# Kernel tuning notes

Measured on AMD Instinct MI355X. Metric: run time of the kernel, lower is better.

Reference implementation:

```python
import jax, jax.numpy as jnp
import numpy as np

TIMESTEPS = 1000
DIFFUSION_SPEED = 0.01
B, N = 4, 2048
E = N * (N - 1) // 2  # strict lower-triangular entries per graph


def _build_Qt():
    # Qt[t-1] = [[1-f, f], [f, 1-f]],  f = 0.5*(1-(1-2s)^t), t = 1..T
    ts = jnp.arange(1, TIMESTEPS + 1, dtype=jnp.float32)
    flip = 0.5 * (1.0 - (1.0 - 2.0 * DIFFUSION_SPEED) ** ts)          # [T]
    row0 = jnp.stack([1.0 - flip, flip], axis=-1)                      # [T,2]
    row1 = jnp.stack([flip, 1.0 - flip], axis=-1)                      # [T,2]
    return jnp.stack([row0, row1], axis=1)                             # [T,2,2]


def setup_inputs() -> dict:
    key = jax.random.key(0)
    k1, k2, k3, k4 = jax.random.split(key, 4)
    adj_start = jax.random.randint(k1, (B, N, N), 0, 2, dtype=jnp.int32)
    t = jax.random.randint(k2, (B,), 0, TIMESTEPS, dtype=jnp.int32)
    u = jax.random.uniform(k3, (B, N, N), dtype=jnp.float32)
    q_approx = jax.random.normal(k4, (B, E), dtype=jnp.float32)
    return {"adj_start": adj_start, "t": t, "u": u, "q_approx": q_approx}


def reference(adj_start, t, u, q_approx):
    Qt = _build_Qt()                                                   # [T,2,2]
    # symmetrize raw adjacency into a binary undirected adjacency
    a = jnp.tril(adj_start, -1)
    adj0 = a + jnp.swapaxes(a, -1, -2)                                 # [B,N,N] in {0,1}

    b_idx = jnp.arange(B)[:, None, None]

    # ---- forward diffusion: sample x_t ~ Categorical(Qt[t][adj0]) ----
    probs = Qt[t][b_idx, adj0]                                         # [B,N,N,2]
    x_t = (u < probs[..., 1]).astype(adj0.dtype)                       # [B,N,N]

    # ---- backward diffusion: q(x_{t-1} | x_t, x_0) ----
    Q_likelihood = Qt[0]                                               # [2,2]
    Q_prior = Qt[t - 1]                                                # [B,2,2] (t=0 wraps, as in torch)
    Q_evidence = Qt[t]                                                 # [B,2,2]

    likelihood = Q_likelihood[x_t]                                     # [B,N,N,2]
    prior = Q_prior[b_idx, adj0]                                       # [B,N,N,2]
    evidence = Q_evidence[b_idx, adj0, x_t]                            # [B,N,N]
    q_backward = likelihood * prior / evidence[..., None]              # [B,N,N,2]

    ti, tj = np.tril_indices(N, -1)                                    # static indices
    q_target = q_backward[:, ti, tj, 1]                                # [B,E]

    # ---- BCE-with-logits loss (mean) ----
    x = q_approx
    loss = jnp.mean(jnp.maximum(x, 0.0) - x * q_target + jnp.log1p(jnp.exp(-jnp.abs(x))))
    return loss
```

## Files before the change

### kernel.cpp

```cpp
#include <hip/hip_runtime.h>
#include <math.h>

#define TIMESTEPS 1000
constexpr int Bc = 4;
constexpr int Nc = 2048;
constexpr long long Ec = (long long)Nc * (Nc - 1) / 2;

__global__ __launch_bounds__(256) void diff_loss_kernel(
    const int* __restrict__ adj, const int* __restrict__ t,
    const float* __restrict__ u, const float* __restrict__ q,
    double* __restrict__ partials)
{
    __shared__ float tab[Bc][8];
    if (threadIdx.x < Bc) {
        int b = threadIdx.x;
        int tb = t[b];
        float f_t = 0.5f * (1.0f - powf(0.98f, (float)(tb + 1)));
        int tpe = (tb == 0) ? TIMESTEPS : tb;
        float f_p = 0.5f * (1.0f - powf(0.98f, (float)tpe));
        float f0  = 0.5f * (1.0f - 0.98f);
        float omf_t = 1.0f - f_t;
        tab[b][0] = f_t;
        tab[b][1] = omf_t;
        tab[b][2] = f0          * f_p          / omf_t;
        tab[b][3] = (1.0f - f0) * f_p          / f_t;
        tab[b][4] = f0          * (1.0f - f_p) / f_t;
        tab[b][5] = (1.0f - f0) * (1.0f - f_p) / omf_t;
    }
    __syncthreads();

    const int totalGroups = Bc * Nc * (Nc / 4);
    const int stride = gridDim.x * blockDim.x;
    double acc = 0.0;
    for (int g = blockIdx.x * blockDim.x + threadIdx.x; g < totalGroups; g += stride) {
        int b   = g >> 20;
        int rem = g & ((1 << 20) - 1);
        int i   = rem >> 9;
        int j0  = (rem & 511) << 2;
        if (j0 >= i) continue;

        long long base = ((long long)b << 22) + (i << 11) + j0;
        const int4   a4 = *(const int4*)(adj + base);
        const float4 u4 = *(const float4*)(u + base);

        float p0   = tab[b][0], p1   = tab[b][1];
        float qt00 = tab[b][2], qt01 = tab[b][3];
        float qt10 = tab[b][4], qt11 = tab[b][5];

        long long e0 = (long long)b * Ec + (((long long)i * (i - 1)) >> 1) + j0;

        int   aa[4] = {a4.x, a4.y, a4.z, a4.w};
        float uu[4] = {u4.x, u4.y, u4.z, u4.w};
        float s = 0.0f;
        #pragma unroll
        for (int k = 0; k < 4; ++k) {
            if (j0 + k < i) {
                int   a0  = aa[k];
                float ps  = a0 ? p1 : p0;
                int   x   = (uu[k] < ps) ? 1 : 0;
                float qtv = a0 ? (x ? qt11 : qt10) : (x ? qt01 : qt00);
                float qv  = q[e0 + k];
                float l = fmaxf(qv, 0.0f) - qv * qtv + log1pf(expf(-fabsf(qv)));
                s += l;
            }
        }
        acc += (double)s;
    }

    for (int off = 32; off > 0; off >>= 1)
        acc += __shfl_down(acc, off, 64);
    __shared__ double wsum[4];
    int lane = threadIdx.x & 63, wid = threadIdx.x >> 6;
    if (lane == 0) wsum[wid] = acc;
    __syncthreads();
    if (threadIdx.x == 0)
        partials[blockIdx.x] = wsum[0] + wsum[1] + wsum[2] + wsum[3];
}

__global__ __launch_bounds__(256) void final_reduce_kernel(
    const double* __restrict__ partials, int nb, float* __restrict__ out)
{
    double acc = 0.0;
    for (int idx = threadIdx.x; idx < nb; idx += blockDim.x)
        acc += partials[idx];
    for (int off = 32; off > 0; off >>= 1)
        acc += __shfl_down(acc, off, 64);
    __shared__ double wsum[4];
    int lane = threadIdx.x & 63, wid = threadIdx.x >> 6;
    if (lane == 0) wsum[wid] = acc;
    __syncthreads();
    if (threadIdx.x == 0)
        out[0] = (float)((wsum[0] + wsum[1] + wsum[2] + wsum[3]) /
                         (double)(Bc * Ec));
}

extern "C" void kernel_launch(void* const* d_in, const int* in_sizes, int n_in,
                              void* d_out, int out_size, void* d_ws, size_t ws_size,
                              hipStream_t stream) {
    const int*   adj = (const int*)d_in[0];
    const int*   t   = (const int*)d_in[1];
    const float* u   = (const float*)d_in[2];
    const float* q   = (const float*)d_in[3];
    float*  out      = (float*)d_out;
    double* partials = (double*)d_ws;

    const int NB = 2048;
    diff_loss_kernel<<<NB, 256, 0, stream>>>(adj, t, u, q, partials);
    final_reduce_kernel<<<1, 256, 0, stream>>>(partials, NB, out);
}
```

Before: 189.1 us.

## Iterate over packed triangular edge index with vectorized q loads

Each thread now handles four consecutive edges of the packed lower-triangular q array instead of four matrix cells. It recovers the row and column with a float sqrt plus integer corrections, loads q as a float4, and loads adj and u as scalars. This removes the idle threads that the old row-major loop spent on the upper triangle and its unaligned scalar q loads. In exchange the adj and u loads become non-vectorized and can cross row boundaries, and log1p/exp are replaced by the fast __logf/__expf intrinsics, which lowers precision.

```diff
diff --git a/kernel.cpp b/kernel.cpp
--- a/kernel.cpp
+++ b/kernel.cpp
@@ -4,7 +4,8 @@
 #define TIMESTEPS 1000
 constexpr int Bc = 4;
 constexpr int Nc = 2048;
-constexpr long long Ec = (long long)Nc * (Nc - 1) / 2;
+constexpr int EcI = Nc * (Nc - 1) / 2;
+constexpr int EG  = EcI / 4;
 
 __global__ __launch_bounds__(256) void diff_loss_kernel(
     const int* __restrict__ adj, const int* __restrict__ t,
@@ -29,40 +30,44 @@
     }
     __syncthreads();
 
-    const int totalGroups = Bc * Nc * (Nc / 4);
+    const int totalEG = Bc * EG;
     const int stride = gridDim.x * blockDim.x;
     double acc = 0.0;
-    for (int g = blockIdx.x * blockDim.x + threadIdx.x; g < totalGroups; g += stride) {
-        int b   = g >> 20;
-        int rem = g & ((1 << 20) - 1);
-        int i   = rem >> 9;
-        int j0  = (rem & 511) << 2;
-        if (j0 >= i) continue;
+    for (int g = blockIdx.x * blockDim.x + threadIdx.x; g < totalEG; g += stride) {
+        int b  = g / EG;
+        int e0 = (g - b * EG) << 2;
 
-        long long base = ((long long)b << 22) + (i << 11) + j0;
-        const int4   a4 = *(const int4*)(adj + base);
-        const float4 u4 = *(const float4*)(u + base);
+        float sf = sqrtf((float)(8 * e0 + 1));
+        int i = (int)((1.0f + sf) * 0.5f);
+        if (i * (i - 1) / 2 > e0)  --i;
+        if (i * (i + 1) / 2 <= e0) ++i;
+        int j = e0 - i * (i - 1) / 2;
 
         float p0   = tab[b][0], p1   = tab[b][1];
         float qt00 = tab[b][2], qt01 = tab[b][3];
         float qt10 = tab[b][4], qt11 = tab[b][5];
 
-        long long e0 = (long long)b * Ec + (((long long)i * (i - 1)) >> 1) + j0;
+        const float4 q4 = *(const float4*)(q + b * EcI + e0);
+        const float qk[4] = {q4.x, q4.y, q4.z, q4.w};
 
-        int   aa[4] = {a4.x, a4.y, a4.z, a4.w};
-        float uu[4] = {u4.x, u4.y, u4.z, u4.w};
+        int ii = i, jj = j;
         float s = 0.0f;
         #pragma unroll
         for (int k = 0; k < 4; ++k) {
-            if (j0 + k < i) {
-                int   a0  = aa[k];
-                float ps  = a0 ? p1 : p0;
-                int   x   = (uu[k] < ps) ? 1 : 0;
-                float qtv = a0 ? (x ? qt11 : qt10) : (x ? qt01 : qt00);
-                float qv  = q[e0 + k];
-                float l = fmaxf(qv, 0.0f) - qv * qtv + log1pf(expf(-fabsf(qv)));
-                s += l;
-            }
+            bool adv = (jj >= ii);
+            ii += adv;
+            jj = adv ? 0 : jj;
+            int base = (b << 22) + (ii << 11) + jj;
+            int   a0 = adj[base];
+            float uu = u[base];
+            float ps  = a0 ? p1 : p0;
+            bool  x   = (uu < ps);
+            float t0  = x ? qt01 : qt00;
+            float t1  = x ? qt11 : qt10;
+            float qtv = a0 ? t1 : t0;
+            float qv  = qk[k];
+            s += fmaxf(qv, 0.0f) - qv * qtv + __logf(1.0f + __expf(-fabsf(qv)));
+            ++jj;
         }
         acc += (double)s;
     }
@@ -91,7 +96,7 @@
     __syncthreads();
     if (threadIdx.x == 0)
         out[0] = (float)((wsum[0] + wsum[1] + wsum[2] + wsum[3]) /
-                         (double)(Bc * Ec));
+                         ((double)Bc * (double)EcI));
 }
 
 extern "C" void kernel_launch(void* const* d_in, const int* in_sizes, int n_in,
```

Result: faster. 164.7 us (-12.9%).
